# Optimization experiments

Hardware: AMD Instinct MI355X
Metric: run time of the kernel (lower is better)

## Reference

```python
import jax, jax.numpy as jnp
import numpy as np

N, E = 50000, 800000
IN, EIN, HID, OUT = 128, 64, 256, 256
L, H = 3, 4
D = HID // H  # per-head out_feats


def setup_inputs() -> dict:
    key = jax.random.key(0)
    ks = jax.random.split(key, 20)
    s = 0.02
    return {
        "h": jax.random.normal(ks[0], (N, IN), jnp.float32),
        "efeat": jax.random.normal(ks[1], (E, EIN), jnp.float32),
        "src": jax.random.randint(ks[2], (E,), 0, N, jnp.int32),
        "dst": jax.random.randint(ks[3], (E,), 0, N, jnp.int32),
        "enc_w": jax.random.normal(ks[4], (IN, HID), jnp.float32) * s,
        "enc_b": jnp.zeros((HID,), jnp.float32),
        "eenc_w": jax.random.normal(ks[5], (EIN, HID), jnp.float32) * s,
        "eenc_b": jnp.zeros((HID,), jnp.float32),
        "Wn": jax.random.normal(ks[6], (L, HID, HID), jnp.float32) * s,
        "We": jax.random.normal(ks[7], (L, HID, HID), jnp.float32) * s,
        "al": jax.random.normal(ks[8], (L, H, D), jnp.float32) * s,
        "ar": jax.random.normal(ks[9], (L, H, D), jnp.float32) * s,
        "ae": jax.random.normal(ks[10], (L, H, D), jnp.float32) * s,
        "ln_g": jnp.ones((L, HID), jnp.float32),
        "ln_b": jnp.zeros((L, HID), jnp.float32),
        "out_w": jax.random.normal(ks[11], (HID, OUT), jnp.float32) * s,
        "out_b": jnp.zeros((OUT,), jnp.float32),
    }


def reference(h, efeat, src, dst, enc_w, enc_b, eenc_w, eenc_b,
              Wn, We, al, ar, ae, ln_g, ln_b, out_w, out_b):
    # Dropout layers act as identity (eval mode).
    n = h.shape[0]
    x = h @ enc_w + enc_b                      # [N, HID] node encoder
    ef = efeat @ eenc_w + eenc_b               # [E, HID] edge encoder
    nl, nh, nd = al.shape
    for l in range(nl):
        res = x
        feat = (x @ Wn[l]).reshape(n, nh, nd)          # [N,H,D]
        eft = (ef @ We[l]).reshape(-1, nh, nd)         # [E,H,D]
        el = jnp.sum(feat * al[l], axis=-1)            # [N,H]
        er = jnp.sum(feat * ar[l], axis=-1)            # [N,H]
        ee = jnp.sum(eft * ae[l], axis=-1)             # [E,H]
        e = jax.nn.leaky_relu(el[src] + er[dst] + ee, 0.2)  # [E,H]
        # edge softmax over incoming edges of each dst node
        m = jax.lax.stop_gradient(jax.ops.segment_max(e, dst, num_segments=n))
        a = jnp.exp(e - m[dst])
        ssum = jax.ops.segment_sum(a, dst, num_segments=n)
        alpha = a / ssum[dst]                          # [E,H]
        agg = jax.ops.segment_sum(alpha[:, :, None] * feat[src], dst,
                                  num_segments=n)      # [N,H,D]
        x = jax.nn.relu(agg.reshape(n, nh * nd))
        y = x + res
        mu = jnp.mean(y, axis=-1, keepdims=True)
        var = jnp.var(y, axis=-1, keepdims=True)
        x = (y - mu) / jnp.sqrt(var + 1e-5) * ln_g[l] + ln_b[l]
    return x @ out_w + out_b
```

## Files before the change

### kernel.cpp

```cpp
#include <hip/hip_runtime.h>
#include <math.h>


typedef __attribute__((ext_vector_type(8))) short bf16x8;
typedef __attribute__((ext_vector_type(8))) unsigned short u16x8;
typedef __attribute__((ext_vector_type(4))) float f32x4;

__device__ __forceinline__ ushort f2b(float f) {
    unsigned u; __builtin_memcpy(&u, &f, 4);
    unsigned r = u + 0x7FFF + ((u >> 16) & 1);
    return (ushort)(r >> 16);
}
__device__ __forceinline__ float b2f(ushort u) {
    unsigned x = (unsigned)u << 16;
    float f; __builtin_memcpy(&f, &x, 4);
    return f;
}

__global__ void k_deg(const int* __restrict__ dst, int* __restrict__ deg, int E) {
    int e = blockIdx.x * 256 + threadIdx.x;
    if (e < E) atomicAdd(&deg[dst[e]], 1);
}

__global__ void k_bsum(const int* __restrict__ deg, int* __restrict__ bsum, int n) {
    __shared__ int wsum[4];
    int tid = threadIdx.x;
    int idx = blockIdx.x * 1024 + tid * 4;
    int4 v = make_int4(0, 0, 0, 0);
    if (idx + 3 < n) v = *(const int4*)(deg + idx);
    else {
        if (idx + 0 < n) v.x = deg[idx + 0];
        if (idx + 1 < n) v.y = deg[idx + 1];
        if (idx + 2 < n) v.z = deg[idx + 2];
    }
    int s = v.x + v.y + v.z + v.w;
#pragma unroll
    for (int off = 32; off; off >>= 1) s += __shfl_down(s, off, 64);
    if ((tid & 63) == 0) wsum[tid >> 6] = s;
    __syncthreads();
    if (tid == 0) bsum[blockIdx.x] = wsum[0] + wsum[1] + wsum[2] + wsum[3];
}

__global__ void k_bscan(const int* __restrict__ bsum, int* __restrict__ boff,
                        int* __restrict__ rowp, int NB, int n) {
    int tid = threadIdx.x;
    int v = (tid < NB) ? bsum[tid] : 0;
    int sc = v;
#pragma unroll
    for (int off = 1; off < 64; off <<= 1) {
        int t = __shfl_up(sc, off, 64);
        if ((tid & 63) >= off) sc += t;
    }
    if (tid < NB) boff[tid] = sc - v;
    if (tid == 63) rowp[n] = sc;
}

__global__ void k_bwrite(const int* __restrict__ deg, const int* __restrict__ boff,
                         int* __restrict__ rowp, int* __restrict__ cursor, int n) {
    __shared__ int wsum[4];
    __shared__ int woff_sh[4];
    int tid = threadIdx.x;
    int lane = tid & 63, wid = tid >> 6;
    int idx = blockIdx.x * 1024 + tid * 4;
    int4 v = make_int4(0, 0, 0, 0);
    if (idx + 3 < n) v = *(const int4*)(deg + idx);
    else {
        if (idx + 0 < n) v.x = deg[idx + 0];
        if (idx + 1 < n) v.y = deg[idx + 1];
        if (idx + 2 < n) v.z = deg[idx + 2];
    }
    int sum4 = v.x + v.y + v.z + v.w;
    int sc = sum4;
#pragma unroll
    for (int off = 1; off < 64; off <<= 1) {
        int t = __shfl_up(sc, off, 64);
        if (lane >= off) sc += t;
    }
    if (lane == 63) wsum[wid] = sc;
    __syncthreads();
    if (tid < 4) {
        int o = 0;
        for (int w = 0; w < tid; w++) o += wsum[w];
        woff_sh[tid] = o;
    }
    __syncthreads();
    int ex = boff[blockIdx.x] + woff_sh[wid] + (sc - sum4);
    int p0 = ex, p1 = ex + v.x, p2 = p1 + v.y, p3 = p2 + v.z;
    if (idx + 0 < n) { rowp[idx + 0] = p0; cursor[idx + 0] = p0; }
    if (idx + 1 < n) { rowp[idx + 1] = p1; cursor[idx + 1] = p1; }
    if (idx + 2 < n) { rowp[idx + 2] = p2; cursor[idx + 2] = p2; }
    if (idx + 3 < n) { rowp[idx + 3] = p3; cursor[idx + 3] = p3; }
}

__global__ void k_scatter(const int* __restrict__ dst, const int* __restrict__ src,
                          int* __restrict__ cursor, int* __restrict__ eid,
                          int* __restrict__ esrc, int E) {
    int e = blockIdx.x * 256 + threadIdx.x;
    if (e < E) {
        int pos = atomicAdd(&cursor[dst[e]], 1);
        eid[pos] = e;
        esrc[pos] = src[e];
    }
}

__global__ void k_ew(const float* __restrict__ We, const float* __restrict__ ae,
                     float* __restrict__ ew) {
    int t = blockIdx.x * 256 + threadIdx.x;
    if (t >= 3072) return;
    int l = t >> 10, r = t & 1023;
    int k = r >> 2, h = r & 3;
    const float* w = We + (size_t)l * 65536 + (size_t)k * 256 + h * 64;
    const float* a = ae + l * 256 + h * 64;
    float s = 0.f;
    for (int d = 0; d < 64; d++) s += w[d] * a[d];
    ew[t] = s;
}

__global__ void k_eew(const float* __restrict__ eenc_w, const float* __restrict__ eenc_b,
                      const float* __restrict__ ew, float* __restrict__ eew2,
                      float* __restrict__ eeb) {
    int t = blockIdx.x * 256 + threadIdx.x;
    if (t < 768) {
        int j = t / 12, lh = t % 12;
        int l = lh >> 2, h = lh & 3;
        float s = 0.f;
        for (int k = 0; k < 256; k++) s += eenc_w[j * 256 + k] * ew[l * 1024 + k * 4 + h];
        eew2[j * 12 + lh] = s;
    } else if (t < 780) {
        int lh = t - 768;
        int l = lh >> 2, h = lh & 3;
        float s = 0.f;
        for (int k = 0; k < 256; k++) s += eenc_b[k] * ew[l * 1024 + k * 4 + h];
        eeb[lh] = s;
    }
}

__global__ __launch_bounds__(256) void k_ee(const float* __restrict__ efeat,
                                            const float* __restrict__ eew2,
                                            const float* __restrict__ eeb,
                                            float* __restrict__ ee_l,
                                            int E) {
    const int tid = threadIdx.x;
    const int lane = tid & 63;
    const int wave = tid >> 6;
    const int q = lane & 7;
    const int g8 = lane >> 3;

    float W[8][12];
#pragma unroll
    for (int u = 0; u < 4; u++)
#pragma unroll
        for (int t = 0; t < 12; t++) {
            W[u][t]     = eew2[(q * 4 + u) * 12 + t];
            W[u + 4][t] = eew2[(32 + q * 4 + u) * 12 + t];
        }
    float Bv[12];
#pragma unroll
    for (int t = 0; t < 12; t++) Bv[t] = eeb[t];

    const int base = blockIdx.x * 128 + wave * 32;
#pragma unroll
    for (int p = 0; p < 4; p++) {
        int e = base + p * 8 + g8;
        if (e >= E) return;
        float4 v0 = *(const float4*)(efeat + (size_t)e * 64 + q * 4);
        float4 v1 = *(const float4*)(efeat + (size_t)e * 64 + 32 + q * 4);
        float acc[12];
#pragma unroll
        for (int t = 0; t < 12; t++)
            acc[t] = v0.x * W[0][t] + v0.y * W[1][t] + v0.z * W[2][t] + v0.w * W[3][t] +
                     v1.x * W[4][t] + v1.y * W[5][t] + v1.z * W[6][t] + v1.w * W[7][t];
#pragma unroll
        for (int m = 1; m < 8; m <<= 1)
#pragma unroll
            for (int t = 0; t < 12; t++) acc[t] += __shfl_xor(acc[t], m, 64);
        if (q == 0) {
#pragma unroll
            for (int l = 0; l < 3; l++) {
                float4 o = make_float4(acc[l * 4 + 0] + Bv[l * 4 + 0],
                                       acc[l * 4 + 1] + Bv[l * 4 + 1],
                                       acc[l * 4 + 2] + Bv[l * 4 + 2],
                                       acc[l * 4 + 3] + Bv[l * 4 + 3]);
                *(float4*)(ee_l + (size_t)l * E * 4 + (size_t)e * 4) = o;
            }
        }
    }
}

__global__ void k_f2b(const float* __restrict__ in, ushort* __restrict__ out, int n4) {
    int i = blockIdx.x * 256 + threadIdx.x;
    if (i >= n4) return;
    float4 v = *(const float4*)(in + (size_t)i * 4);
    ushort4 o;
    o.x = f2b(v.x); o.y = f2b(v.y); o.z = f2b(v.z); o.w = f2b(v.w);
    *(ushort4*)(out + (size_t)i * 4) = o;
}

__global__ void k_trs(const float* __restrict__ enc_w, const float* __restrict__ Wn,
                      const float* __restrict__ out_w, ushort* __restrict__ encT,
                      ushort* __restrict__ WnT, ushort* __restrict__ outT) {
    int t = blockIdx.x * 256 + threadIdx.x;
    if (t < 32768) {
        int nn = t >> 7, k = t & 127;
        encT[t] = f2b(enc_w[k * 256 + nn]);
        return;
    }
    t -= 32768;
    if (t < 3 * 65536) {
        int l = t >> 16, r = t & 65535;
        int nn = r >> 8, k = r & 255;
        WnT[(size_t)l * 65536 + r] = f2b(Wn[(size_t)l * 65536 + k * 256 + nn]);
        return;
    }
    t -= 3 * 65536;
    {
        int nn = t >> 8, k = t & 255;
        outT[t] = f2b(out_w[k * 256 + nn]);
    }
}

template <int KTILES, bool BIAS, bool STORE_F32, bool STORE_BF16>
__global__ __launch_bounds__(256) void gemm_mfma(const ushort* __restrict__ A,
                                                 const ushort* __restrict__ BT,
                                                 const float* __restrict__ bias,
                                                 float* __restrict__ Cf,
                                                 ushort* __restrict__ Cb, int M) {
    constexpr int K = KTILES * 32;
    __shared__ __align__(16) ushort As[128 * 32];
    __shared__ __align__(16) ushort Bs[128 * 32];
    const int tid = threadIdx.x;
    const int wave = tid >> 6;
    const int lane = tid & 63;
    const int rowBase = blockIdx.x * 128;
    const int colBase = blockIdx.y * 128;
    const int sRow = lane >> 2;
    const int sCol = (lane & 3) * 8;
    const int c0 = wave * 2, c1 = wave * 2 + 1;

    const ushort* gA0 = A + (size_t)(rowBase + c0 * 16 + sRow) * K + sCol;
    const ushort* gA1 = A + (size_t)(rowBase + c1 * 16 + sRow) * K + sCol;
    const ushort* gB0 = BT + (size_t)(colBase + c0 * 16 + sRow) * K + sCol;
    const ushort* gB1 = BT + (size_t)(colBase + c1 * 16 + sRow) * K + sCol;
    ushort* lA0 = As + c0 * 512;
    ushort* lA1 = As + c1 * 512;
    ushort* lB0 = Bs + c0 * 512;
    ushort* lB1 = Bs + c1 * 512;

    f32x4 acc[4][4] = {};
    const int wr = (wave >> 1) * 64, wc = (wave & 1) * 64;
    const int ml = lane & 15, q = lane >> 4;

    for (int kt = 0; kt < KTILES; ++kt) {
        __builtin_amdgcn_global_load_lds(
            (const __attribute__((address_space(1))) unsigned*)(gA0 + kt * 32),
            (__attribute__((address_space(3))) unsigned*)lA0, 16, 0, 0);
        __builtin_amdgcn_global_load_lds(
            (const __attribute__((address_space(1))) unsigned*)(gA1 + kt * 32),
            (__attribute__((address_space(3))) unsigned*)lA1, 16, 0, 0);
        __builtin_amdgcn_global_load_lds(
            (const __attribute__((address_space(1))) unsigned*)(gB0 + kt * 32),
            (__attribute__((address_space(3))) unsigned*)lB0, 16, 0, 0);
        __builtin_amdgcn_global_load_lds(
            (const __attribute__((address_space(1))) unsigned*)(gB1 + kt * 32),
            (__attribute__((address_space(3))) unsigned*)lB1, 16, 0, 0);
        __syncthreads();
        bf16x8 af[4], bfr[4];
#pragma unroll
        for (int i = 0; i < 4; i++)
            af[i] = *(const bf16x8*)&As[(wr + i * 16 + ml) * 32 + q * 8];
#pragma unroll
        for (int j = 0; j < 4; j++)
            bfr[j] = *(const bf16x8*)&Bs[(wc + j * 16 + ml) * 32 + q * 8];
#pragma unroll
        for (int i = 0; i < 4; i++)
#pragma unroll
            for (int j = 0; j < 4; j++)
                acc[i][j] = __builtin_amdgcn_mfma_f32_16x16x32_bf16(af[i], bfr[j], acc[i][j],
                                                                    0, 0, 0);
        __syncthreads();
    }

#pragma unroll
    for (int j = 0; j < 4; j++) {
        const int col = colBase + wc + j * 16 + ml;
        const float bb = BIAS ? bias[col] : 0.f;
#pragma unroll
        for (int i = 0; i < 4; i++) {
#pragma unroll
            for (int r = 0; r < 4; r++) {
                const int row = rowBase + wr + i * 16 + q * 4 + r;
                if (row < M) {
                    float v = acc[i][j][r] + bb;
                    if (STORE_F32) Cf[(size_t)row * 256 + col] = v;
                    if (STORE_BF16) Cb[(size_t)row * 256 + col] = f2b(v);
                }
            }
        }
    }
}

__global__ __launch_bounds__(256) void k_elr(const ushort* __restrict__ feat,
                                             const float* __restrict__ al,
                                             const float* __restrict__ ar,
                                             float* __restrict__ el,
                                             float* __restrict__ er, int N) {
    int lane = threadIdx.x & 63;
    int n = blockIdx.x * 4 + (threadIdx.x >> 6);
    if (n >= N) return;
    ushort4 f4 = *(const ushort4*)&feat[(size_t)n * 256 + lane * 4];
    float4 a4 = *(const float4*)&al[lane * 4];
    float4 r4 = *(const float4*)&ar[lane * 4];
    float f0 = b2f(f4.x), f1 = b2f(f4.y), f2 = b2f(f4.z), f3 = b2f(f4.w);
    float va = f0 * a4.x + f1 * a4.y + f2 * a4.z + f3 * a4.w;
    float vr = f0 * r4.x + f1 * r4.y + f2 * r4.z + f3 * r4.w;
#pragma unroll
    for (int m = 1; m < 16; m <<= 1) {
        va += __shfl_xor(va, m, 64);
        vr += __shfl_xor(vr, m, 64);
    }
    if ((lane & 15) == 0) {
        int h = lane >> 4;
        el[n * 4 + h] = va;
        er[n * 4 + h] = vr;
    }
}

template <bool WRITE_X>
__global__ __launch_bounds__(128) void k_agg(const int* __restrict__ rowp,
                                             const int* __restrict__ eid,
                                             const int* __restrict__ esrc,
                                             const float* __restrict__ ee,
                                             const float* __restrict__ el,
                                             const float* __restrict__ er,
                                             const ushort* __restrict__ feat,
                                             float* __restrict__ x_io,
                                             ushort* __restrict__ xb,
                                             const float* __restrict__ g,
                                             const float* __restrict__ b) {
    const int n = blockIdx.x;
    const int t = threadIdx.x;
    const int start = rowp[n], end = rowp[n + 1];
    __shared__ float w_sh[64][4];
    __shared__ int src_sh[64];
    __shared__ float redA[3][32][8];

    float ern[4];
    if (t < 64) {
        float4 e4 = *(const float4*)(er + (size_t)n * 4);
        ern[0] = e4.x; ern[1] = e4.y; ern[2] = e4.z; ern[3] = e4.w;
    }
    float wsum[4] = {0.f, 0.f, 0.f, 0.f};
    float acc[8] = {0.f, 0.f, 0.f, 0.f, 0.f, 0.f, 0.f, 0.f};
    const int stream = t >> 5;
    const int c = t & 31;
    const int h = c >> 3;

    for (int cs = start; cs < end; cs += 64) {
        if (t < 64 && cs + t < end) {
            int pos = cs + t;
            int e = eid[pos];
            int s = esrc[pos];
            src_sh[t] = s;
            float4 elv = *(const float4*)(el + (size_t)s * 4);
            float4 eev = *(const float4*)(ee + (size_t)e * 4);
            float elva[4] = {elv.x, elv.y, elv.z, elv.w};
            float eeva[4] = {eev.x, eev.y, eev.z, eev.w};
#pragma unroll
            for (int hh = 0; hh < 4; hh++) {
                float sc = elva[hh] + ern[hh] + eeva[hh];
                sc = (sc > 0.f) ? sc : 0.2f * sc;
                float w = __expf(sc);
                w_sh[t][hh] = w;
                wsum[hh] += w;
            }
        }
        __syncthreads();
        int cnt = min(64, end - cs);
        for (int j = stream; j < cnt; j += 4) {
            float w = w_sh[j][h];
            u16x8 p = *(const u16x8*)&feat[(size_t)src_sh[j] * 256 + c * 8];
#pragma unroll
            for (int u = 0; u < 8; u++) acc[u] += w * b2f((ushort)p[u]);
        }
        __syncthreads();
    }

    if (stream > 0) {
#pragma unroll
        for (int u = 0; u < 8; u++) redA[stream - 1][c][u] = acc[u];
    }
    if (t < 64) {
#pragma unroll
        for (int m = 1; m < 64; m <<= 1)
#pragma unroll
            for (int hh = 0; hh < 4; hh++) wsum[hh] += __shfl_xor(wsum[hh], m, 64);
    }
    __syncthreads();
    if (t < 32) {
#pragma unroll
        for (int ss = 0; ss < 3; ss++)
#pragma unroll
            for (int u = 0; u < 8; u++) acc[u] += redA[ss][c][u];
        float4 xr0 = *(const float4*)&x_io[(size_t)n * 256 + c * 8];
        float4 xr1 = *(const float4*)&x_io[(size_t)n * 256 + c * 8 + 4];
        float xra[8] = {xr0.x, xr0.y, xr0.z, xr0.w, xr1.x, xr1.y, xr1.z, xr1.w};
        float inv = (end > start) ? 1.f / wsum[h] : 0.f;
        float y[8];
        float s1 = 0.f, s2 = 0.f;
#pragma unroll
        for (int u = 0; u < 8; u++) {
            float v = fmaxf(acc[u] * inv, 0.f);
            y[u] = v + xra[u];
            s1 += y[u];
            s2 += y[u] * y[u];
        }
#pragma unroll
        for (int m = 1; m < 32; m <<= 1) {
            s1 += __shfl_xor(s1, m, 64);
            s2 += __shfl_xor(s2, m, 64);
        }
        float mu = s1 * (1.f / 256.f);
        float var = s2 * (1.f / 256.f) - mu * mu;
        float rstd = rsqrtf(var + 1e-5f);
        float4 gv0 = *(const float4*)&g[c * 8];
        float4 gv1 = *(const float4*)&g[c * 8 + 4];
        float4 bv0 = *(const float4*)&b[c * 8];
        float4 bv1 = *(const float4*)&b[c * 8 + 4];
        float ga[8] = {gv0.x, gv0.y, gv0.z, gv0.w, gv1.x, gv1.y, gv1.z, gv1.w};
        float ba[8] = {bv0.x, bv0.y, bv0.z, bv0.w, bv1.x, bv1.y, bv1.z, bv1.w};
        float o[8];
        u16x8 ob;
#pragma unroll
        for (int u = 0; u < 8; u++) {
            o[u] = (y[u] - mu) * rstd * ga[u] + ba[u];
            ob[u] = f2b(o[u]);
        }
        if (WRITE_X) {
            *(float4*)&x_io[(size_t)n * 256 + c * 8] =
                make_float4(o[0], o[1], o[2], o[3]);
            *(float4*)&x_io[(size_t)n * 256 + c * 8 + 4] =
                make_float4(o[4], o[5], o[6], o[7]);
        }
        *(u16x8*)&xb[(size_t)n * 256 + c * 8] = ob;
    }
}

extern "C" void kernel_launch(void* const* d_in, const int* in_sizes, int n_in,
                              void* d_out, int out_size, void* d_ws, size_t ws_size,
                              hipStream_t stream) {
    const float* h      = (const float*)d_in[0];
    const float* efeat  = (const float*)d_in[1];
    const int*   src    = (const int*)d_in[2];
    const int*   dst    = (const int*)d_in[3];
    const float* enc_w  = (const float*)d_in[4];
    const float* enc_b  = (const float*)d_in[5];
    const float* eenc_w = (const float*)d_in[6];
    const float* eenc_b = (const float*)d_in[7];
    const float* Wn     = (const float*)d_in[8];
    const float* We     = (const float*)d_in[9];
    const float* al     = (const float*)d_in[10];
    const float* ar     = (const float*)d_in[11];
    const float* ae     = (const float*)d_in[12];
    const float* ln_g   = (const float*)d_in[13];
    const float* ln_b   = (const float*)d_in[14];
    const float* out_w  = (const float*)d_in[15];
    const float* out_b  = (const float*)d_in[16];

    const int N = in_sizes[0] / 128;
    const int E = in_sizes[2];
    const int Mpad = ((N + 127) / 128) * 128;
    const int NB = (N + 1023) / 1024;

    char* ws = (char*)d_ws;
    size_t off = 0;
    auto alloc = [&](size_t bytes) -> char* {
        char* p = ws + off;
        off += (bytes + 255) & ~(size_t)255;
        return p;
    };
    float*  X      = (float*)alloc((size_t)Mpad * 256 * 4);
    ushort* Xb     = (ushort*)alloc((size_t)Mpad * 256 * 2);
    ushort* F      = (ushort*)alloc((size_t)Mpad * 256 * 2);
    ushort* hb     = (ushort*)alloc((size_t)Mpad * 128 * 2);
    float*  el     = (float*)alloc((size_t)N * 4 * 4);
    float*  er     = (float*)alloc((size_t)N * 4 * 4);
    float*  ee_l   = (float*)alloc((size_t)E * 12 * 4);
    int*    esrc   = (int*)alloc((size_t)E * 4);
    int*    eid    = (int*)alloc((size_t)E * 4);
    int*    deg    = (int*)alloc((size_t)N * 4);
    int*    rowp   = (int*)alloc((size_t)(N + 1) * 4);
    int*    cursor = (int*)alloc((size_t)N * 4);
    int*    bsum   = (int*)alloc(64 * 4);
    int*    boff   = (int*)alloc(64 * 4);
    float*  ew     = (float*)alloc(3072 * 4);
    float*  eew2   = (float*)alloc(768 * 4);
    float*  eeb    = (float*)alloc(64);
    ushort* encT   = (ushort*)alloc(256 * 128 * 2);
    ushort* WnT    = (ushort*)alloc(3 * 256 * 256 * 2);
    ushort* outT   = (ushort*)alloc(256 * 256 * 2);
    (void)ws_size; (void)n_in; (void)out_size;

    hipMemsetAsync(deg, 0, (size_t)N * 4, stream);
    k_deg<<<(E + 255) / 256, 256, 0, stream>>>(dst, deg, E);
    k_bsum<<<NB, 256, 0, stream>>>(deg, bsum, N);
    k_bscan<<<1, 64, 0, stream>>>(bsum, boff, rowp, NB, N);
    k_bwrite<<<NB, 256, 0, stream>>>(deg, boff, rowp, cursor, N);
    k_scatter<<<(E + 255) / 256, 256, 0, stream>>>(dst, src, cursor, eid, esrc, E);

    k_ew<<<12, 256, 0, stream>>>(We, ae, ew);
    k_eew<<<4, 256, 0, stream>>>(eenc_w, eenc_b, ew, eew2, eeb);
    k_ee<<<(E + 127) / 128, 256, 0, stream>>>(efeat, eew2, eeb, ee_l, E);

    k_f2b<<<(N * 128 / 4 + 255) / 256, 256, 0, stream>>>(h, hb, N * 128 / 4);
    k_trs<<<(32768 + 4 * 65536 + 255) / 256, 256, 0, stream>>>(enc_w, Wn, out_w,
                                                               encT, WnT, outT);

    dim3 gG(Mpad / 128, 2);
    gemm_mfma<4, true, true, true><<<gG, 256, 0, stream>>>(hb, encT, enc_b, X, Xb, N);

    for (int l = 0; l < 3; l++) {
        gemm_mfma<8, false, false, true><<<gG, 256, 0, stream>>>(
            Xb, WnT + (size_t)l * 65536, nullptr, nullptr, F, N);
        k_elr<<<(N + 3) / 4, 256, 0, stream>>>(F, al + l * 256, ar + l * 256, el, er, N);
        if (l < 2)
            k_agg<true><<<N, 128, 0, stream>>>(rowp, eid, esrc, ee_l + (size_t)l * E * 4,
                                               el, er, F, X, Xb, ln_g + l * 256,
                                               ln_b + l * 256);
        else
            k_agg<false><<<N, 128, 0, stream>>>(rowp, eid, esrc, ee_l + (size_t)l * E * 4,
                                                el, er, F, X, Xb, ln_g + l * 256,
                                                ln_b + l * 256);
    }
    gemm_mfma<8, true, true, false><<<gG, 256, 0, stream>>>(Xb, outT, out_b,
                                                            (float*)d_out, nullptr, N);
}
```

Measured before the change: 886.9 us.

## Store edge scores in CSR order and aggregate one node per wave

The scatter kernel now records each edge's CSR position, and the edge-score kernel writes its per-layer scores directly in CSR order. This removes the eid indirection and the random ee gather in aggregation. Aggregation is restructured so each 64-lane wave handles one destination node end to end, with no block barriers and a wave-wide LayerNorm reduction, in place of a 128-thread block per node. The fp32-to-bf16 input conversion and the weight transposes are also fused into one prep kernel. The trade-off is that each wave now walks its neighbour edges serially, so high-degree nodes could cause load imbalance.

```diff
diff --git a/kernel.cpp b/kernel.cpp
--- a/kernel.cpp
+++ b/kernel.cpp
@@ -3,7 +3,6 @@
 
 
 typedef __attribute__((ext_vector_type(8))) short bf16x8;
-typedef __attribute__((ext_vector_type(8))) unsigned short u16x8;
 typedef __attribute__((ext_vector_type(4))) float f32x4;
 
 __device__ __forceinline__ ushort f2b(float f) {
@@ -93,12 +92,12 @@
 }
 
 __global__ void k_scatter(const int* __restrict__ dst, const int* __restrict__ src,
-                          int* __restrict__ cursor, int* __restrict__ eid,
+                          int* __restrict__ cursor, int* __restrict__ perm,
                           int* __restrict__ esrc, int E) {
     int e = blockIdx.x * 256 + threadIdx.x;
     if (e < E) {
         int pos = atomicAdd(&cursor[dst[e]], 1);
-        eid[pos] = e;
+        perm[e] = pos;
         esrc[pos] = src[e];
     }
 }
@@ -138,6 +137,7 @@
 __global__ __launch_bounds__(256) void k_ee(const float* __restrict__ efeat,
                                             const float* __restrict__ eew2,
                                             const float* __restrict__ eeb,
+                                            const int* __restrict__ perm,
                                             float* __restrict__ ee_l,
                                             int E) {
     const int tid = threadIdx.x;
@@ -175,31 +175,32 @@
 #pragma unroll
             for (int t = 0; t < 12; t++) acc[t] += __shfl_xor(acc[t], m, 64);
         if (q == 0) {
+            int pos = perm[e];
 #pragma unroll
             for (int l = 0; l < 3; l++) {
                 float4 o = make_float4(acc[l * 4 + 0] + Bv[l * 4 + 0],
                                        acc[l * 4 + 1] + Bv[l * 4 + 1],
                                        acc[l * 4 + 2] + Bv[l * 4 + 2],
                                        acc[l * 4 + 3] + Bv[l * 4 + 3]);
-                *(float4*)(ee_l + (size_t)l * E * 4 + (size_t)e * 4) = o;
+                *(float4*)(ee_l + (size_t)l * E * 4 + (size_t)pos * 4) = o;
             }
         }
     }
 }
 
-__global__ void k_f2b(const float* __restrict__ in, ushort* __restrict__ out, int n4) {
-    int i = blockIdx.x * 256 + threadIdx.x;
-    if (i >= n4) return;
-    float4 v = *(const float4*)(in + (size_t)i * 4);
-    ushort4 o;
-    o.x = f2b(v.x); o.y = f2b(v.y); o.z = f2b(v.z); o.w = f2b(v.w);
-    *(ushort4*)(out + (size_t)i * 4) = o;
-}
-
-__global__ void k_trs(const float* __restrict__ enc_w, const float* __restrict__ Wn,
-                      const float* __restrict__ out_w, ushort* __restrict__ encT,
-                      ushort* __restrict__ WnT, ushort* __restrict__ outT) {
+__global__ void k_prep(const float* __restrict__ h, const float* __restrict__ enc_w,
+                       const float* __restrict__ Wn, const float* __restrict__ out_w,
+                       ushort* __restrict__ hb, ushort* __restrict__ encT,
+                       ushort* __restrict__ WnT, ushort* __restrict__ outT, int n4) {
     int t = blockIdx.x * 256 + threadIdx.x;
+    if (t < n4) {
+        float4 v = *(const float4*)(h + (size_t)t * 4);
+        ushort4 o;
+        o.x = f2b(v.x); o.y = f2b(v.y); o.z = f2b(v.z); o.w = f2b(v.w);
+        *(ushort4*)(hb + (size_t)t * 4) = o;
+        return;
+    }
+    t -= n4;
     if (t < 32768) {
         int nn = t >> 7, k = t & 127;
         encT[t] = f2b(enc_w[k * 256 + nn]);
@@ -213,7 +214,7 @@
         return;
     }
     t -= 3 * 65536;
-    {
+    if (t < 65536) {
         int nn = t >> 8, k = t & 255;
         outT[t] = f2b(out_w[k * 256 + nn]);
     }
@@ -326,8 +327,7 @@
 }
 
 template <bool WRITE_X>
-__global__ __launch_bounds__(128) void k_agg(const int* __restrict__ rowp,
-                                             const int* __restrict__ eid,
+__global__ __launch_bounds__(256) void k_agg(const int* __restrict__ rowp,
                                              const int* __restrict__ esrc,
                                              const float* __restrict__ ee,
                                              const float* __restrict__ el,
@@ -336,113 +336,92 @@
                                              float* __restrict__ x_io,
                                              ushort* __restrict__ xb,
                                              const float* __restrict__ g,
-                                             const float* __restrict__ b) {
-    const int n = blockIdx.x;
-    const int t = threadIdx.x;
+                                             const float* __restrict__ b, int N) {
+    __shared__ float w_sh[4][64][4];
+    __shared__ int s_sh[4][64];
+    const int wv = threadIdx.x >> 6;
+    const int lane = threadIdx.x & 63;
+    const int n = blockIdx.x * 4 + wv;
+    if (n >= N) return;
     const int start = rowp[n], end = rowp[n + 1];
-    __shared__ float w_sh[64][4];
-    __shared__ int src_sh[64];
-    __shared__ float redA[3][32][8];
-
-    float ern[4];
-    if (t < 64) {
-        float4 e4 = *(const float4*)(er + (size_t)n * 4);
-        ern[0] = e4.x; ern[1] = e4.y; ern[2] = e4.z; ern[3] = e4.w;
-    }
+    const int h = lane >> 4;
+
+    float4 e4 = *(const float4*)(er + (size_t)n * 4);
+    float ern[4] = {e4.x, e4.y, e4.z, e4.w};
     float wsum[4] = {0.f, 0.f, 0.f, 0.f};
-    float acc[8] = {0.f, 0.f, 0.f, 0.f, 0.f, 0.f, 0.f, 0.f};
-    const int stream = t >> 5;
-    const int c = t & 31;
-    const int h = c >> 3;
+    float acc[4] = {0.f, 0.f, 0.f, 0.f};
 
     for (int cs = start; cs < end; cs += 64) {
-        if (t < 64 && cs + t < end) {
-            int pos = cs + t;
-            int e = eid[pos];
+        const int m = min(64, end - cs);
+        if (lane < m) {
+            int pos = cs + lane;
             int s = esrc[pos];
-            src_sh[t] = s;
+            s_sh[wv][lane] = s;
+            float4 eev = *(const float4*)(ee + (size_t)pos * 4);
             float4 elv = *(const float4*)(el + (size_t)s * 4);
-            float4 eev = *(const float4*)(ee + (size_t)e * 4);
-            float elva[4] = {elv.x, elv.y, elv.z, elv.w};
-            float eeva[4] = {eev.x, eev.y, eev.z, eev.w};
+            float ea[4] = {eev.x, eev.y, eev.z, eev.w};
+            float la[4] = {elv.x, elv.y, elv.z, elv.w};
 #pragma unroll
             for (int hh = 0; hh < 4; hh++) {
-                float sc = elva[hh] + ern[hh] + eeva[hh];
+                float sc = la[hh] + ern[hh] + ea[hh];
                 sc = (sc > 0.f) ? sc : 0.2f * sc;
                 float w = __expf(sc);
-                w_sh[t][hh] = w;
+                w_sh[wv][lane][hh] = w;
                 wsum[hh] += w;
             }
         }
-        __syncthreads();
-        int cnt = min(64, end - cs);
-        for (int j = stream; j < cnt; j += 4) {
-            float w = w_sh[j][h];
-            u16x8 p = *(const u16x8*)&feat[(size_t)src_sh[j] * 256 + c * 8];
-#pragma unroll
-            for (int u = 0; u < 8; u++) acc[u] += w * b2f((ushort)p[u]);
+        asm volatile("s_waitcnt lgkmcnt(0)" ::: "memory");
+        __builtin_amdgcn_sched_barrier(0);
+        for (int j = 0; j < m; ++j) {
+            int s = s_sh[wv][j];
+            float w = w_sh[wv][j][h];
+            ushort4 p = *(const ushort4*)&feat[(size_t)s * 256 + lane * 4];
+            acc[0] += w * b2f(p.x);
+            acc[1] += w * b2f(p.y);
+            acc[2] += w * b2f(p.z);
+            acc[3] += w * b2f(p.w);
         }
-        __syncthreads();
-    }
-
-    if (stream > 0) {
-#pragma unroll
-        for (int u = 0; u < 8; u++) redA[stream - 1][c][u] = acc[u];
-    }
-    if (t < 64) {
-#pragma unroll
-        for (int m = 1; m < 64; m <<= 1)
-#pragma unroll
-            for (int hh = 0; hh < 4; hh++) wsum[hh] += __shfl_xor(wsum[hh], m, 64);
-    }
-    __syncthreads();
-    if (t < 32) {
-#pragma unroll
-        for (int ss = 0; ss < 3; ss++)
-#pragma unroll
-            for (int u = 0; u < 8; u++) acc[u] += redA[ss][c][u];
-        float4 xr0 = *(const float4*)&x_io[(size_t)n * 256 + c * 8];
-        float4 xr1 = *(const float4*)&x_io[(size_t)n * 256 + c * 8 + 4];
-        float xra[8] = {xr0.x, xr0.y, xr0.z, xr0.w, xr1.x, xr1.y, xr1.z, xr1.w};
-        float inv = (end > start) ? 1.f / wsum[h] : 0.f;
-        float y[8];
-        float s1 = 0.f, s2 = 0.f;
-#pragma unroll
-        for (int u = 0; u < 8; u++) {
-            float v = fmaxf(acc[u] * inv, 0.f);
-            y[u] = v + xra[u];
-            s1 += y[u];
-            s2 += y[u] * y[u];
-        }
-#pragma unroll
-        for (int m = 1; m < 32; m <<= 1) {
-            s1 += __shfl_xor(s1, m, 64);
-            s2 += __shfl_xor(s2, m, 64);
-        }
-        float mu = s1 * (1.f / 256.f);
-        float var = s2 * (1.f / 256.f) - mu * mu;
-        float rstd = rsqrtf(var + 1e-5f);
-        float4 gv0 = *(const float4*)&g[c * 8];
-        float4 gv1 = *(const float4*)&g[c * 8 + 4];
-        float4 bv0 = *(const float4*)&b[c * 8];
-        float4 bv1 = *(const float4*)&b[c * 8 + 4];
-        float ga[8] = {gv0.x, gv0.y, gv0.z, gv0.w, gv1.x, gv1.y, gv1.z, gv1.w};
-        float ba[8] = {bv0.x, bv0.y, bv0.z, bv0.w, bv1.x, bv1.y, bv1.z, bv1.w};
-        float o[8];
-        u16x8 ob;
-#pragma unroll
-        for (int u = 0; u < 8; u++) {
-            o[u] = (y[u] - mu) * rstd * ga[u] + ba[u];
-            ob[u] = f2b(o[u]);
-        }
-        if (WRITE_X) {
-            *(float4*)&x_io[(size_t)n * 256 + c * 8] =
-                make_float4(o[0], o[1], o[2], o[3]);
-            *(float4*)&x_io[(size_t)n * 256 + c * 8 + 4] =
-                make_float4(o[4], o[5], o[6], o[7]);
-        }
-        *(u16x8*)&xb[(size_t)n * 256 + c * 8] = ob;
-    }
+        asm volatile("s_waitcnt lgkmcnt(0)" ::: "memory");
+        __builtin_amdgcn_sched_barrier(0);
+    }
+
+#pragma unroll
+    for (int mm = 1; mm < 64; mm <<= 1)
+#pragma unroll
+        for (int hh = 0; hh < 4; hh++) wsum[hh] += __shfl_xor(wsum[hh], mm, 64);
+
+    float inv = (end > start) ? 1.f / wsum[h] : 0.f;
+    float4 xr = *(const float4*)&x_io[(size_t)n * 256 + lane * 4];
+    float xra[4] = {xr.x, xr.y, xr.z, xr.w};
+    float y[4];
+    float s1 = 0.f, s2 = 0.f;
+#pragma unroll
+    for (int u = 0; u < 4; u++) {
+        float v = fmaxf(acc[u] * inv, 0.f);
+        y[u] = v + xra[u];
+        s1 += y[u];
+        s2 += y[u] * y[u];
+    }
+#pragma unroll
+    for (int mm = 1; mm < 64; mm <<= 1) {
+        s1 += __shfl_xor(s1, mm, 64);
+        s2 += __shfl_xor(s2, mm, 64);
+    }
+    float mu = s1 * (1.f / 256.f);
+    float var = s2 * (1.f / 256.f) - mu * mu;
+    float rstd = rsqrtf(var + 1e-5f);
+    float4 gv = *(const float4*)&g[lane * 4];
+    float4 bv = *(const float4*)&b[lane * 4];
+    float ga[4] = {gv.x, gv.y, gv.z, gv.w};
+    float ba[4] = {bv.x, bv.y, bv.z, bv.w};
+    float o[4];
+    ushort4 ob;
+#pragma unroll
+    for (int u = 0; u < 4; u++) o[u] = (y[u] - mu) * rstd * ga[u] + ba[u];
+    ob.x = f2b(o[0]); ob.y = f2b(o[1]); ob.z = f2b(o[2]); ob.w = f2b(o[3]);
+    if (WRITE_X)
+        *(float4*)&x_io[(size_t)n * 256 + lane * 4] = make_float4(o[0], o[1], o[2], o[3]);
+    *(ushort4*)&xb[(size_t)n * 256 + lane * 4] = ob;
 }
 
 extern "C" void kernel_launch(void* const* d_in, const int* in_sizes, int n_in,
@@ -486,7 +465,7 @@
     float*  er     = (float*)alloc((size_t)N * 4 * 4);
     float*  ee_l   = (float*)alloc((size_t)E * 12 * 4);
     int*    esrc   = (int*)alloc((size_t)E * 4);
-    int*    eid    = (int*)alloc((size_t)E * 4);
+    int*    perm   = (int*)alloc((size_t)E * 4);
     int*    deg    = (int*)alloc((size_t)N * 4);
     int*    rowp   = (int*)alloc((size_t)(N + 1) * 4);
     int*    cursor = (int*)alloc((size_t)N * 4);
@@ -505,15 +484,15 @@
     k_bsum<<<NB, 256, 0, stream>>>(deg, bsum, N);
     k_bscan<<<1, 64, 0, stream>>>(bsum, boff, rowp, NB, N);
     k_bwrite<<<NB, 256, 0, stream>>>(deg, boff, rowp, cursor, N);
-    k_scatter<<<(E + 255) / 256, 256, 0, stream>>>(dst, src, cursor, eid, esrc, E);
+    k_scatter<<<(E + 255) / 256, 256, 0, stream>>>(dst, src, cursor, perm, esrc, E);
 
     k_ew<<<12, 256, 0, stream>>>(We, ae, ew);
     k_eew<<<4, 256, 0, stream>>>(eenc_w, eenc_b, ew, eew2, eeb);
-    k_ee<<<(E + 127) / 128, 256, 0, stream>>>(efeat, eew2, eeb, ee_l, E);
-
-    k_f2b<<<(N * 128 / 4 + 255) / 256, 256, 0, stream>>>(h, hb, N * 128 / 4);
-    k_trs<<<(32768 + 4 * 65536 + 255) / 256, 256, 0, stream>>>(enc_w, Wn, out_w,
-                                                               encT, WnT, outT);
+    k_ee<<<(E + 127) / 128, 256, 0, stream>>>(efeat, eew2, eeb, perm, ee_l, E);
+
+    const int n4 = N * 128 / 4;
+    k_prep<<<(n4 + 32768 + 4 * 65536 + 255) / 256, 256, 0, stream>>>(
+        h, enc_w, Wn, out_w, hb, encT, WnT, outT, n4);
 
     dim3 gG(Mpad / 128, 2);
     gemm_mfma<4, true, true, true><<<gG, 256, 0, stream>>>(hb, encT, enc_b, X, Xb, N);
@@ -523,13 +502,13 @@
             Xb, WnT + (size_t)l * 65536, nullptr, nullptr, F, N);
         k_elr<<<(N + 3) / 4, 256, 0, stream>>>(F, al + l * 256, ar + l * 256, el, er, N);
         if (l < 2)
-            k_agg<true><<<N, 128, 0, stream>>>(rowp, eid, esrc, ee_l + (size_t)l * E * 4,
-                                               el, er, F, X, Xb, ln_g + l * 256,
-                                               ln_b + l * 256);
+            k_agg<true><<<(N + 3) / 4, 256, 0, stream>>>(rowp, esrc,
+                ee_l + (size_t)l * E * 4, el, er, F, X, Xb, ln_g + l * 256,
+                ln_b + l * 256, N);
         else
-            k_agg<false><<<N, 128, 0, stream>>>(rowp, eid, esrc, ee_l + (size_t)l * E * 4,
-                                                el, er, F, X, Xb, ln_g + l * 256,
-                                                ln_b + l * 256);
+            k_agg<false><<<(N + 3) / 4, 256, 0, stream>>>(rowp, esrc,
+                ee_l + (size_t)l * E * 4, el, er, F, X, Xb, ln_g + l * 256,
+                ln_b + l * 256, N);
     }
     gemm_mfma<8, true, true, false><<<gG, 256, 0, stream>>>(Xb, outT, out_b,
                                                             (float*)d_out, nullptr, N);
```

New measurement: 887.3 us. Within noise of the previous version (+0.0%).
